# Kernel tuning notes

Measured on AMD Instinct MI355X. Metric: run time of the kernel, lower is better.

Reference implementation:

```python
import jax, jax.numpy as jnp
import numpy as np

QMIN, QMAX = -128.0, 127.0  # int8 range


def _fake_int_cast(t):
    # Emulates .to(torch.int8) on an already-clamped float tensor:
    # truncation toward zero, then back to float.
    return jnp.trunc(t)


def setup_inputs() -> dict:
    key = jax.random.key(0)
    k_x, k_w, k_ws, k_is, k_b = jax.random.split(key, 5)
    B, S, IN, OUT = 4, 2048, 4096, 4096
    x = jax.random.normal(k_x, (B, S, IN), dtype=jnp.float32)
    # quant_weight buffer holds int8 values (stored here as fp32 integers),
    # produced by quantizing a dense fp weight with per-out-channel scales.
    weight_scale = jax.random.uniform(k_ws, (OUT, 1), dtype=jnp.float32, minval=0.005, maxval=0.02)
    w_fp = jax.random.normal(k_w, (OUT, IN), dtype=jnp.float32) * 0.02
    quant_weight = jnp.trunc(jnp.clip(w_fp / weight_scale, QMIN, QMAX))
    input_scale = jax.random.uniform(k_is, (1,), dtype=jnp.float32, minval=0.01, maxval=0.03)
    bias = jax.random.normal(k_b, (OUT,), dtype=jnp.float32)
    return {"x": x, "quant_weight": quant_weight, "weight_scale": weight_scale,
            "input_scale": input_scale, "bias": bias}


def reference(x, quant_weight, weight_scale, input_scale, bias):
    # quantize input: clamp(x/scale) -> int8 (trunc toward zero) -> float
    quant_input = _fake_int_cast(jnp.clip(x / input_scale, QMIN, QMAX))
    # int8 matmul performed in fp32: [B,S,IN] @ [OUT,IN]^T -> [B,S,OUT]
    quant_output = jnp.einsum("bsi,oi->bso", quant_input, quant_weight)
    # dequantize with combined per-out-channel scale, viewed [1,1,OUT]
    scale = (weight_scale * input_scale).reshape((1,) * (quant_output.ndim - 1) + (-1,))
    output = quant_output * scale
    output = output + bias
    return output
```

## Files before the change

kernel.cpp:

```cpp
#include <hip/hip_runtime.h>


using v4i = __attribute__((ext_vector_type(4))) int;

typedef const __attribute__((address_space(1))) signed char gc_t;
typedef __attribute__((address_space(3))) signed char lc_t;

constexpr int BM = 128;
constexpr int BN = 128;
constexpr int BK = 128;


__device__ __forceinline__ int quant4(const float4 f, float s) {
    int a = (int)fminf(fmaxf(f.x / s, -128.0f), 127.0f);
    int b = (int)fminf(fmaxf(f.y / s, -128.0f), 127.0f);
    int c = (int)fminf(fmaxf(f.z / s, -128.0f), 127.0f);
    int d = (int)fminf(fmaxf(f.w / s, -128.0f), 127.0f);
    return (a & 0xff) | ((b & 0xff) << 8) | ((c & 0xff) << 16) | ((d & 0xff) << 24);
}

__global__ void quant_x_kernel(const float4* __restrict__ x,
                               const float* __restrict__ scale,
                               int* __restrict__ out, int n4) {
    const float s = scale[0];
    int i = blockIdx.x * blockDim.x + threadIdx.x;
    if (i >= n4) return;
    out[i] = quant4(x[i], s);
}

__global__ void quant_w_kernel(const float4* __restrict__ w,
                               int* __restrict__ out, int n4) {
    int i = blockIdx.x * blockDim.x + threadIdx.x;
    if (i >= n4) return;
    float4 f = w[i];
    out[i] = ((int)f.x & 0xff) | (((int)f.y & 0xff) << 8) |
             (((int)f.z & 0xff) << 16) | (((int)f.w & 0xff) << 24);
}


__global__ __launch_bounds__(256, 4) void gemm_i8_kernel(
    const signed char* __restrict__ Aq,
    const signed char* __restrict__ Wq,
    const float* __restrict__ wscale,
    const float* __restrict__ iscale,
    const float* __restrict__ bias,
    float* __restrict__ C,
    int M, int N, int K)
{
    __shared__ signed char As[BM * BK];
    __shared__ signed char Bs[BN * BK];

    const int tid  = threadIdx.x;
    const int wave = tid >> 6;
    const int lane = tid & 63;
    const int wm   = (wave >> 1) * 64;
    const int wn   = (wave & 1) * 64;

    const int m0 = blockIdx.y * BM;
    const int n0 = blockIdx.x * BN;

    const int srow = lane >> 3;
    const int gchunk = (lane & 7) ^ srow;

    const int fr = lane & 15;
    const int qh = lane >> 4;
    const int coff0 = (((0 * 4) + qh) ^ (fr & 7)) * 16;
    const int coff1 = (((1 * 4) + qh) ^ (fr & 7)) * 16;

    v4i acc[4][4];
#pragma unroll
    for (int i = 0; i < 4; ++i)
#pragma unroll
        for (int j = 0; j < 4; ++j) acc[i][j] = (v4i){0, 0, 0, 0};

    const size_t Kz = (size_t)K;
    const signed char* pA = Aq + (size_t)(m0 + wave * 32 + srow) * Kz + gchunk * 16;
    const signed char* pB = Wq + (size_t)(n0 + wave * 32 + srow) * Kz + gchunk * 16;
    lc_t* lA = (lc_t*)(As + (wave * 32) * BK);
    lc_t* lB = (lc_t*)(Bs + (wave * 32) * BK);

    for (int k0 = 0; k0 < K; k0 += BK) {
#pragma unroll
        for (int c = 0; c < 4; ++c) {
            __builtin_amdgcn_global_load_lds((gc_t*)(pA + (size_t)(c * 8) * Kz),
                                             lA + c * 8 * BK, 16, 0, 0);
            __builtin_amdgcn_global_load_lds((gc_t*)(pB + (size_t)(c * 8) * Kz),
                                             lB + c * 8 * BK, 16, 0, 0);
        }
        pA += BK;
        pB += BK;
        __syncthreads();

#pragma unroll
        for (int s = 0; s < 2; ++s) {
            const int coff = s ? coff1 : coff0;
            v4i af[4], bf[4];
#pragma unroll
            for (int t = 0; t < 4; ++t)
                af[t] = *(const v4i*)(As + (wm + t * 16 + fr) * BK + coff);
#pragma unroll
            for (int t = 0; t < 4; ++t)
                bf[t] = *(const v4i*)(Bs + (wn + t * 16 + fr) * BK + coff);
#pragma unroll
            for (int mt = 0; mt < 4; ++mt)
#pragma unroll
                for (int nt = 0; nt < 4; ++nt)
                    acc[mt][nt] = __builtin_amdgcn_mfma_i32_16x16x64_i8(
                        af[mt], bf[nt], acc[mt][nt], 0, 0, 0);
        }
        __syncthreads();
    }

    const float is = iscale[0];
#pragma unroll
    for (int nt = 0; nt < 4; ++nt) {
        const int col = n0 + wn + nt * 16 + fr;
        const float sc = wscale[col] * is;
        const float bv = bias[col];
#pragma unroll
        for (int mt = 0; mt < 4; ++mt) {
            const int rbase = m0 + wm + mt * 16 + qh * 4;
#pragma unroll
            for (int r = 0; r < 4; ++r) {
                C[(size_t)(rbase + r) * N + col] = (float)acc[mt][nt][r] * sc + bv;
            }
        }
    }
}


extern "C" void kernel_launch(void* const* d_in, const int* in_sizes, int n_in,
                              void* d_out, int out_size, void* d_ws, size_t ws_size,
                              hipStream_t stream) {
    const float* x  = (const float*)d_in[0];
    const float* qw = (const float*)d_in[1];
    const float* ws = (const float*)d_in[2];
    const float* is = (const float*)d_in[3];
    const float* bs = (const float*)d_in[4];
    float* out = (float*)d_out;

    const int nx = in_sizes[0];
    const int nw = in_sizes[1];
    const int N  = in_sizes[4];
    const int K  = nw / N;
    const int M  = nx / K;

    signed char* xq = (signed char*)d_ws;
    signed char* wq = (signed char*)d_ws + (size_t)nx;

    quant_x_kernel<<<nx / 4 / 256, 256, 0, stream>>>(
        (const float4*)x, is, (int*)xq, nx / 4);
    quant_w_kernel<<<nw / 4 / 256, 256, 0, stream>>>(
        (const float4*)qw, (int*)wq, nw / 4);

    dim3 grid(N / BN, M / BM);
    gemm_i8_kernel<<<grid, 256, 0, stream>>>(xq, wq, ws, is, bs, out, M, N, K);
}
```

Measured before the change: 378.3 us.

## Enlarge GEMM tile to 256x256 with double-buffered LDS prefetch and XCD remap

Raises the int8 GEMM tile from 128x128 to 256x256 with 8 waves per block, each wave owning a 128x64 sub-tile. Shared memory is double-buffered, and the tile two steps ahead is prefetched with global_load_lds while the current one is computed, using explicit vmcnt waits, barriers and setprio around the MFMA bursts. Block indices are remapped across 8 XCD groups to improve L2 locality. The aim is to hide global load latency and raise arithmetic intensity, at the cost of 128KB of LDS per block, a larger accumulator register footprint and fewer blocks per CU.

```diff
diff --git a/kernel.cpp b/kernel.cpp
--- a/kernel.cpp
+++ b/kernel.cpp
@@ -6,9 +6,10 @@
 typedef const __attribute__((address_space(1))) signed char gc_t;
 typedef __attribute__((address_space(3))) signed char lc_t;
 
-constexpr int BM = 128;
-constexpr int BN = 128;
+constexpr int BM = 256;
+constexpr int BN = 256;
 constexpr int BK = 128;
+constexpr int TILE_BYTES = BM * BK;
 
 
 __device__ __forceinline__ int quant4(const float4 f, float s) {
@@ -38,7 +39,26 @@
 }
 
 
-__global__ __launch_bounds__(256, 4) void gemm_i8_kernel(
+#define STAGE_TILE(dstbuf, kbyte)                                              \
+    do {                                                                       \
+        const signed char* _pa = pA + (size_t)(kbyte);                         \
+        const signed char* _pb = pB + (size_t)(kbyte);                         \
+        lc_t* _la = (lc_t*)(smem + (dstbuf) * (2 * TILE_BYTES) +               \
+                            (wid * 8) * BK);                                   \
+        lc_t* _lb = (lc_t*)(smem + (dstbuf) * (2 * TILE_BYTES) + TILE_BYTES +  \
+                            (wid * 8) * BK);                                   \
+        _Pragma("unroll")                                                      \
+        for (int c = 0; c < 4; ++c) {                                          \
+            __builtin_amdgcn_global_load_lds(                                  \
+                (gc_t*)(_pa + (size_t)(c * 64) * Kz), _la + c * 64 * BK,       \
+                16, 0, 0);                                                     \
+            __builtin_amdgcn_global_load_lds(                                  \
+                (gc_t*)(_pb + (size_t)(c * 64) * Kz), _lb + c * 64 * BK,       \
+                16, 0, 0);                                                     \
+        }                                                                      \
+    } while (0)
+
+__global__ __launch_bounds__(512, 2) void gemm_i8_kernel(
     const signed char* __restrict__ Aq,
     const signed char* __restrict__ Wq,
     const float* __restrict__ wscale,
@@ -47,68 +67,97 @@
     float* __restrict__ C,
     int M, int N, int K)
 {
-    __shared__ signed char As[BM * BK];
-    __shared__ signed char Bs[BN * BK];
+    __shared__ signed char smem[2 * 2 * TILE_BYTES];
 
     const int tid  = threadIdx.x;
-    const int wave = tid >> 6;
+    const int wid  = tid >> 6;
     const int lane = tid & 63;
-    const int wm   = (wave >> 1) * 64;
-    const int wn   = (wave & 1) * 64;
-
-    const int m0 = blockIdx.y * BM;
-    const int n0 = blockIdx.x * BN;
-
-    const int srow = lane >> 3;
+    const int wm   = (wid >> 2) * 128;
+    const int wn   = (wid & 3) * 64;
+
+    const int nwg = gridDim.x;
+    int wg = blockIdx.x;
+    if ((nwg & 7) == 0) wg = (wg & 7) * (nwg >> 3) + (wg >> 3);
+    const int ntx = N / BN;
+    const int m0 = (wg / ntx) * BM;
+    const int n0 = (wg % ntx) * BN;
+
+    const int srow   = lane >> 3;
     const int gchunk = (lane & 7) ^ srow;
 
     const int fr = lane & 15;
     const int qh = lane >> 4;
-    const int coff0 = (((0 * 4) + qh) ^ (fr & 7)) * 16;
-    const int coff1 = (((1 * 4) + qh) ^ (fr & 7)) * 16;
-
-    v4i acc[4][4];
-#pragma unroll
-    for (int i = 0; i < 4; ++i)
+    const int coff0 = ((0 * 4 + qh) ^ (fr & 7)) * 16;
+    const int coff1 = ((1 * 4 + qh) ^ (fr & 7)) * 16;
+
+    v4i acc[8][4];
+#pragma unroll
+    for (int i = 0; i < 8; ++i)
 #pragma unroll
         for (int j = 0; j < 4; ++j) acc[i][j] = (v4i){0, 0, 0, 0};
 
     const size_t Kz = (size_t)K;
-    const signed char* pA = Aq + (size_t)(m0 + wave * 32 + srow) * Kz + gchunk * 16;
-    const signed char* pB = Wq + (size_t)(n0 + wave * 32 + srow) * Kz + gchunk * 16;
-    lc_t* lA = (lc_t*)(As + (wave * 32) * BK);
-    lc_t* lB = (lc_t*)(Bs + (wave * 32) * BK);
-
-    for (int k0 = 0; k0 < K; k0 += BK) {
-#pragma unroll
-        for (int c = 0; c < 4; ++c) {
-            __builtin_amdgcn_global_load_lds((gc_t*)(pA + (size_t)(c * 8) * Kz),
-                                             lA + c * 8 * BK, 16, 0, 0);
-            __builtin_amdgcn_global_load_lds((gc_t*)(pB + (size_t)(c * 8) * Kz),
-                                             lB + c * 8 * BK, 16, 0, 0);
-        }
-        pA += BK;
-        pB += BK;
-        __syncthreads();
-
-#pragma unroll
-        for (int s = 0; s < 2; ++s) {
-            const int coff = s ? coff1 : coff0;
-            v4i af[4], bf[4];
-#pragma unroll
-            for (int t = 0; t < 4; ++t)
-                af[t] = *(const v4i*)(As + (wm + t * 16 + fr) * BK + coff);
-#pragma unroll
-            for (int t = 0; t < 4; ++t)
-                bf[t] = *(const v4i*)(Bs + (wn + t * 16 + fr) * BK + coff);
-#pragma unroll
-            for (int mt = 0; mt < 4; ++mt)
-#pragma unroll
-                for (int nt = 0; nt < 4; ++nt)
-                    acc[mt][nt] = __builtin_amdgcn_mfma_i32_16x16x64_i8(
-                        af[mt], bf[nt], acc[mt][nt], 0, 0, 0);
-        }
-        __syncthreads();
+    const signed char* pA = Aq + (size_t)(m0 + wid * 8 + srow) * Kz + gchunk * 16;
+    const signed char* pB = Wq + (size_t)(n0 + wid * 8 + srow) * Kz + gchunk * 16;
+
+    const int NT = K / BK;
+
+    STAGE_TILE(0, 0);
+    STAGE_TILE(1, BK);
+
+    for (int t = 0; t < NT; ++t) {
+        const int cur = t & 1;
+        if (t + 1 < NT) {
+            asm volatile("s_waitcnt vmcnt(8)" ::: "memory");
+        } else {
+            asm volatile("s_waitcnt vmcnt(0)" ::: "memory");
+        }
+        __builtin_amdgcn_s_barrier();
+
+        const signed char* Ab = smem + cur * (2 * TILE_BYTES);
+        const signed char* Bb = Ab + TILE_BYTES;
+
+        v4i bf[4][2];
+        v4i af[2][2];
+
+#pragma unroll
+        for (int p = 0; p < 4; ++p) {
+            if (p == 0) {
+#pragma unroll
+                for (int nt = 0; nt < 4; ++nt) {
+                    const signed char* br = Bb + (size_t)(wn + nt * 16 + fr) * BK;
+                    bf[nt][0] = *(const v4i*)(br + coff0);
+                    bf[nt][1] = *(const v4i*)(br + coff1);
+                }
+            }
+#pragma unroll
+            for (int i = 0; i < 2; ++i) {
+                const signed char* ar =
+                    Ab + (size_t)(wm + (2 * p + i) * 16 + fr) * BK;
+                af[i][0] = *(const v4i*)(ar + coff0);
+                af[i][1] = *(const v4i*)(ar + coff1);
+            }
+            __builtin_amdgcn_s_barrier();
+            __builtin_amdgcn_sched_barrier(0);
+            __builtin_amdgcn_s_setprio(1);
+#pragma unroll
+            for (int s = 0; s < 2; ++s)
+#pragma unroll
+                for (int i = 0; i < 2; ++i)
+#pragma unroll
+                    for (int nt = 0; nt < 4; ++nt)
+                        acc[2 * p + i][nt] = __builtin_amdgcn_mfma_i32_16x16x64_i8(
+                            af[i][s], bf[nt][s], acc[2 * p + i][nt], 0, 0, 0);
+            __builtin_amdgcn_s_setprio(0);
+            __builtin_amdgcn_sched_barrier(0);
+            __builtin_amdgcn_s_barrier();
+        }
+
+        if (t + 2 < NT) {
+            asm volatile("" ::: "memory");
+            STAGE_TILE(cur, (size_t)(t + 2) * BK);
+            asm volatile("" ::: "memory");
+        }
     }
 
     const float is = iscale[0];
@@ -118,11 +167,11 @@
         const float sc = wscale[col] * is;
         const float bv = bias[col];
 #pragma unroll
-        for (int mt = 0; mt < 4; ++mt) {
-            const int rbase = m0 + wm + mt * 16 + qh * 4;
+        for (int mt = 0; mt < 8; ++mt) {
+            const size_t rbase = (size_t)(m0 + wm + mt * 16 + qh * 4);
 #pragma unroll
             for (int r = 0; r < 4; ++r) {
-                C[(size_t)(rbase + r) * N + col] = (float)acc[mt][nt][r] * sc + bv;
+                C[(rbase + r) * N + col] = (float)acc[mt][nt][r] * sc + bv;
             }
         }
     }
@@ -153,6 +202,6 @@
     quant_w_kernel<<<nw / 4 / 256, 256, 0, stream>>>(
         (const float4*)qw, (int*)wq, nw / 4);
 
-    dim3 grid(N / BN, M / BM);
-    gemm_i8_kernel<<<grid, 256, 0, stream>>>(xq, wq, ws, is, bs, out, M, N, K);
-}
+    dim3 grid((M / BM) * (N / BN));
+    gemm_i8_kernel<<<grid, 512, 0, stream>>>(xq, wq, ws, is, bs, out, M, N, K);
+}
```

After: 411.7 us. 8.8% more time.
